# Kernel tuning notes

Hardware: AMD Instinct MI355X
Metric: run time of the kernel (lower is better)

## Reference

```python
import jax, jax.numpy as jnp
import numpy as np


def setup_inputs() -> dict:
    key = jax.random.key(0)
    k1, k2 = jax.random.split(key)
    N, B, H, W, ks = 2048, 64, 4096, 4096, 8
    grid = H // B  # 64 block positions per axis
    block_indices = jax.random.randint(k1, (N, 2), 0, grid, dtype=jnp.int64)
    block_values = jax.random.normal(k2, (N, B, B, ks), dtype=jnp.float32)
    return {
        "block_values": block_values,
        "block_indices": block_indices,
        "block_size": B,
        "H": H,
        "W": W,
        "ks": ks,
    }


def reference(block_values, block_indices, block_size, H, W, ks):
    """Fused scatter-add equivalent of BlockSparseTensor.to_dense().

    block_values:  [N, B, B, ks] float
    block_indices: [N, 2] int (block row, block col)
    returns dense [H, W, ks], summing overlapping blocks and clipping at edges.
    """
    B = block_size
    offs = jnp.arange(B)
    rows = block_indices[:, 0:1] * B + offs  # [N, B] absolute row indices
    cols = block_indices[:, 1:2] * B + offs  # [N, B] absolute col indices
    # boundary clipping: zero contributions that fall outside (H, W)
    mask = (rows[:, :, None] < H) & (cols[:, None, :] < W)  # [N, B, B]
    vals = jnp.where(mask[..., None], block_values, jnp.zeros((), block_values.dtype))
    dense = jnp.zeros((H, W, ks), dtype=block_values.dtype)
    # broadcasting indices [N,B,1] x [N,1,B] -> scatter-add of [N,B,B,ks]
    dense = dense.at[rows[:, :, None], cols[:, None, :]].add(vals, mode="drop")
    return dense
```

## Files before the change

### kernel.cpp

```cpp
#include <hip/hip_runtime.h>

#define GRIDN 64
#define NCELLS 4096
#define BVEC 8192
#define ROWSTRIDE4 8192

typedef float f32x4 __attribute__((ext_vector_type(4)));

__global__ __launch_bounds__(256) void k_fused(const int* __restrict__ idxw,
                                               const f32x4* __restrict__ bv4,
                                               f32x4* __restrict__ out4,
                                               int N) {
    const int cell = blockIdx.x >> 2;
    const int chunk = blockIdx.x & 3;
    const int R = cell >> 6;
    const int C = cell & (GRIDN - 1);
    const int tid = threadIdx.x;
    const int w = tid >> 6;
    const int lane = tid & 63;

    __shared__ unsigned long long masks[32];
    __shared__ short list_s[2048];
    __shared__ int odd_or;
    __shared__ int cnt_s;

    if (tid == 0) { odd_or = 0; cnt_s = 0; }
    __syncthreads();

    int my_or = 0;
#pragma unroll
    for (int k = 0; k < 8; ++k) {
        const int n = w * 512 + k * 64 + lane;
        int2 p = ((const int2*)idxw)[n];
        my_or |= p.y;
        const bool match = (n < N) && (p.x == R) && (p.y == C);
        unsigned long long mk = __ballot(match);
        if (lane == 0) masks[w * 8 + k] = mk;
    }
    if (__any(my_or != 0) && lane == 0) odd_or = 1;
    __syncthreads();

    if (odd_or == 0) {
#pragma unroll
        for (int k = 0; k < 8; ++k) {
            const int n = w * 512 + k * 64 + lane;
            int4 p = ((const int4*)idxw)[n];
            const bool match = (n < N) && (p.x == R) && (p.z == C);
            unsigned long long mk = __ballot(match);
            if (lane == 0) masks[w * 8 + k] = mk;
        }
        __syncthreads();
    }

    if (tid < 64) {
        unsigned long long mk = (lane < 32) ? masks[lane] : 0ULL;
        const int pc = __popcll(mk);
        int pre = pc;
#pragma unroll
        for (int d = 1; d < 32; d <<= 1) {
            int v = __shfl_up(pre, d, 64);
            if (lane >= d) pre += v;
        }
        int pos = pre - pc;
        const int base = lane * 64;
        while (mk) {
            const int b = __ffsll(mk) - 1;
            list_s[pos++] = (short)(base + b);
            mk &= mk - 1;
        }
        if (lane == 31) cnt_s = pre;
    }
    __syncthreads();
    const int cnt = cnt_s;

    const int tbase = chunk * 2048 + tid;
    const size_t obase = (size_t)(R * 64) * ROWSTRIDE4 + (size_t)C * 128;

    if (cnt == 0) {
        const f32x4 z = {0.f, 0.f, 0.f, 0.f};
#pragma unroll
        for (int i = 0; i < 8; ++i) {
            int t = tbase + i * 256;
            __builtin_nontemporal_store(z, &out4[obase + (size_t)(t >> 7) * ROWSTRIDE4 + (t & 127)]);
        }
    } else if (cnt == 1) {
        const f32x4* __restrict__ src = bv4 + (size_t)list_s[0] * BVEC;
#pragma unroll
        for (int i = 0; i < 8; ++i) {
            int t = tbase + i * 256;
            f32x4 v = __builtin_nontemporal_load(&src[t]);
            __builtin_nontemporal_store(v, &out4[obase + (size_t)(t >> 7) * ROWSTRIDE4 + (t & 127)]);
        }
    } else {
        f32x4 acc[8];
#pragma unroll
        for (int i = 0; i < 8; ++i) acc[i] = (f32x4){0.f, 0.f, 0.f, 0.f};
        for (int j = 0; j < cnt; ++j) {
            const f32x4* __restrict__ src = bv4 + (size_t)list_s[j] * BVEC;
#pragma unroll
            for (int i = 0; i < 8; ++i)
                acc[i] += __builtin_nontemporal_load(&src[tbase + i * 256]);
        }
#pragma unroll
        for (int i = 0; i < 8; ++i) {
            int t = tbase + i * 256;
            __builtin_nontemporal_store(acc[i], &out4[obase + (size_t)(t >> 7) * ROWSTRIDE4 + (t & 127)]);
        }
    }
}

extern "C" void kernel_launch(void* const* d_in, const int* in_sizes, int n_in,
                              void* d_out, int out_size, void* d_ws, size_t ws_size,
                              hipStream_t stream) {
    const float* bv = (const float*)d_in[0];
    const int* idxw = (const int*)d_in[1];
    const int N = in_sizes[1] / 2;

    k_fused<<<NCELLS * 4, 256, 0, stream>>>(idxw, (const f32x4*)bv,
                                            (f32x4*)d_out, N);
}
```

Measured before the change: 157.6 us.

## Precompute per-cell block counts and cell ids in a setup kernel

Adds a single-block setup kernel that works out whether indices are int64, converts each block index to a 16-bit cell id, and histograms per-cell counts into workspace. The dense kernel reads its cell count first, so empty cells write zeros right away without scanning all N indices, and non-empty cells scan compact 16-bit ids instead of the raw index pairs. The cost is an extra serial launch with one 1024-thread block on the critical path, plus shared-memory atomics.

```diff
diff --git a/kernel.cpp b/kernel.cpp
--- a/kernel.cpp
+++ b/kernel.cpp
@@ -5,9 +5,47 @@
 #define BVEC 8192
 #define ROWSTRIDE4 8192
 
+#define WS_CNT 0
+#define WS_CID 4096
+
 typedef float f32x4 __attribute__((ext_vector_type(4)));
 
-__global__ __launch_bounds__(256) void k_fused(const int* __restrict__ idxw,
+__global__ __launch_bounds__(1024) void k_setup(const int* __restrict__ idxw,
+                                                int N, int* __restrict__ ws_i) {
+    __shared__ int counts_s[NCELLS];
+    __shared__ int f64_s;
+    const int tid = threadIdx.x;
+
+    int local = 0;
+    for (int i = 1 + 2 * tid; i < 2 * N; i += 2048) local |= idxw[i];
+    if (tid == 0) f64_s = 0;
+    for (int i = tid; i < NCELLS; i += 1024) counts_s[i] = 0;
+    __syncthreads();
+    if (local) f64_s = 1;
+    __syncthreads();
+    const int is64 = (f64_s == 0);
+
+    unsigned short* cid = (unsigned short*)(ws_i + WS_CID);
+    for (int n = tid; n < N; n += 1024) {
+        int r, c;
+        if (is64) {
+            const long long* p = (const long long*)idxw;
+            r = (int)p[2 * n];
+            c = (int)p[2 * n + 1];
+        } else {
+            r = idxw[2 * n];
+            c = idxw[2 * n + 1];
+        }
+        int cell = (r >= 0 && r < GRIDN && c >= 0 && c < GRIDN) ? r * GRIDN + c
+                                                                : 0xFFFF;
+        cid[n] = (unsigned short)cell;
+        if (cell != 0xFFFF) atomicAdd(&counts_s[cell], 1);
+    }
+    __syncthreads();
+    for (int i = tid; i < NCELLS; i += 1024) ws_i[WS_CNT + i] = counts_s[i];
+}
+
+__global__ __launch_bounds__(256) void k_dense(const int* __restrict__ ws_i,
                                                const f32x4* __restrict__ bv4,
                                                f32x4* __restrict__ out4,
                                                int N) {
@@ -16,41 +54,35 @@
     const int R = cell >> 6;
     const int C = cell & (GRIDN - 1);
     const int tid = threadIdx.x;
+    const int tbase = chunk * 2048 + tid;
+    const size_t obase = (size_t)(R * 64) * ROWSTRIDE4 + (size_t)C * 128;
+    const int cnt = ws_i[WS_CNT + cell];
+
+    if (cnt == 0) {
+        const f32x4 z = {0.f, 0.f, 0.f, 0.f};
+#pragma unroll
+        for (int i = 0; i < 8; ++i) {
+            int t = tbase + i * 256;
+            __builtin_nontemporal_store(z, &out4[obase + (size_t)(t >> 7) * ROWSTRIDE4 + (t & 127)]);
+        }
+        return;
+    }
+
     const int w = tid >> 6;
     const int lane = tid & 63;
-
     __shared__ unsigned long long masks[32];
     __shared__ short list_s[2048];
-    __shared__ int odd_or;
-    __shared__ int cnt_s;
+    __shared__ int cnt_chk;
 
-    if (tid == 0) { odd_or = 0; cnt_s = 0; }
-    __syncthreads();
-
-    int my_or = 0;
+    const unsigned short* cid = (const unsigned short*)(ws_i + WS_CID);
 #pragma unroll
     for (int k = 0; k < 8; ++k) {
         const int n = w * 512 + k * 64 + lane;
-        int2 p = ((const int2*)idxw)[n];
-        my_or |= p.y;
-        const bool match = (n < N) && (p.x == R) && (p.y == C);
+        const bool match = (n < N) && ((int)cid[n] == cell);
         unsigned long long mk = __ballot(match);
         if (lane == 0) masks[w * 8 + k] = mk;
     }
-    if (__any(my_or != 0) && lane == 0) odd_or = 1;
     __syncthreads();
-
-    if (odd_or == 0) {
-#pragma unroll
-        for (int k = 0; k < 8; ++k) {
-            const int n = w * 512 + k * 64 + lane;
-            int4 p = ((const int4*)idxw)[n];
-            const bool match = (n < N) && (p.x == R) && (p.z == C);
-            unsigned long long mk = __ballot(match);
-            if (lane == 0) masks[w * 8 + k] = mk;
-        }
-        __syncthreads();
-    }
 
     if (tid < 64) {
         unsigned long long mk = (lane < 32) ? masks[lane] : 0ULL;
@@ -68,22 +100,10 @@
             list_s[pos++] = (short)(base + b);
             mk &= mk - 1;
         }
-        if (lane == 31) cnt_s = pre;
     }
     __syncthreads();
-    const int cnt = cnt_s;
 
-    const int tbase = chunk * 2048 + tid;
-    const size_t obase = (size_t)(R * 64) * ROWSTRIDE4 + (size_t)C * 128;
-
-    if (cnt == 0) {
-        const f32x4 z = {0.f, 0.f, 0.f, 0.f};
-#pragma unroll
-        for (int i = 0; i < 8; ++i) {
-            int t = tbase + i * 256;
-            __builtin_nontemporal_store(z, &out4[obase + (size_t)(t >> 7) * ROWSTRIDE4 + (t & 127)]);
-        }
-    } else if (cnt == 1) {
+    if (cnt == 1) {
         const f32x4* __restrict__ src = bv4 + (size_t)list_s[0] * BVEC;
 #pragma unroll
         for (int i = 0; i < 8; ++i) {
@@ -116,6 +136,9 @@
     const int* idxw = (const int*)d_in[1];
     const int N = in_sizes[1] / 2;
 
-    k_fused<<<NCELLS * 4, 256, 0, stream>>>(idxw, (const f32x4*)bv,
+    int* ws_i = (int*)d_ws;
+
+    k_setup<<<1, 1024, 0, stream>>>(idxw, N, ws_i);
+    k_dense<<<NCELLS * 4, 256, 0, stream>>>(ws_i, (const f32x4*)bv,
                                             (f32x4*)d_out, N);
 }
```

Measured after the change: 169.7 us. 7.7% more time.
